# Optimization experiments

Measured on AMD Instinct MI355X. Metric: run time of the kernel, lower is better.

## Reference

```python
import jax, jax.numpy as jnp
import numpy as np

MAXHD, MAXV, MINA, MAXA, DT = 100.0, 40.0, -6.0, 4.0, 0.1
NVEH, NT, IN_DIM, UNITS = 4096, 1024, 12, 20


def setup_inputs() -> dict:
    key = jax.random.key(0)
    ks = jax.random.split(key, 12)
    leadfol_inputs = jax.random.normal(ks[0], (NVEH, NT, IN_DIM), dtype=jnp.float32)
    init_state = jax.random.normal(ks[1], (NVEH, 2), dtype=jnp.float32)
    hidden_states = jnp.zeros((2, NVEH, UNITS), dtype=jnp.float32)
    s = 0.1
    return {
        "leadfol_inputs": leadfol_inputs,
        "init_state": init_state,
        "hidden_states": hidden_states,
        "kernel": s * jax.random.normal(ks[2], (IN_DIM, 4 * UNITS), dtype=jnp.float32),
        "rkernel": s * jax.random.normal(ks[3], (UNITS, 4 * UNITS), dtype=jnp.float32),
        "bias": jnp.zeros((4 * UNITS,), dtype=jnp.float32),
        "W2": s * jax.random.normal(ks[4], (UNITS, 10), dtype=jnp.float32),
        "b2": jnp.zeros((10,), dtype=jnp.float32),
        "Wlc": s * jax.random.normal(ks[5], (10, 3), dtype=jnp.float32),
        "blc": jnp.zeros((3,), dtype=jnp.float32),
        "W1": s * jax.random.normal(ks[6], (10, 1), dtype=jnp.float32),
        "b1": jnp.zeros((1,), dtype=jnp.float32),
    }


def reference(leadfol_inputs, init_state, hidden_states, kernel, rkernel, bias,
              W2, b2, Wlc, blc, W1, b1):
    # time-major for scan: (nt, nveh, 12)
    xs = jnp.transpose(leadfol_inputs, (1, 0, 2))
    pos0, spd0 = init_state[:, 0], init_state[:, 1]
    h0, c0 = hidden_states[0], hidden_states[1]

    def step(carry, x_t):
        pos, spd, h, c = carry
        lead_hd = (x_t[:, :3] - pos[:, None]) / MAXHD
        fol_hd = (pos[:, None] - x_t[:, 3:6]) / MAXHD
        spds = x_t[:, 6:] / MAXV
        inp = jnp.concatenate([lead_hd, fol_hd, spds], axis=1)  # (nveh, 12)
        inp = jnp.where(jnp.isnan(inp), jnp.ones_like(inp), inp)
        # Keras LSTMCell (inference, no dropout): gate order i, f, g, o
        z = inp @ kernel + h @ rkernel + bias
        i_g, f_g, g_g, o_g = jnp.split(z, 4, axis=1)
        c_new = jax.nn.sigmoid(f_g) * c + jax.nn.sigmoid(i_g) * jnp.tanh(g_g)
        h_new = jax.nn.sigmoid(o_g) * jnp.tanh(c_new)
        x2 = jax.nn.relu(h_new @ W2 + b2)          # (nveh, 10)
        lc = x2 @ Wlc + blc                          # (nveh, 3)
        acc_raw = (x2 @ W1 + b1)[:, 0]               # (nveh,)
        acc = (MAXA - MINA) * acc_raw + MINA
        pos_new = pos + DT * spd
        spd_new = spd + DT * acc
        return (pos_new, spd_new, h_new, c_new), (pos_new, lc)

    (pos_f, spd_f, h_f, c_f), (traj, lc_all) = jax.lax.scan(step, (pos0, spd0, h0, c0), xs)
    pred_traj = jnp.transpose(traj, (1, 0))            # (nveh, nt)
    pred_lc_action = jnp.transpose(lc_all, (1, 0, 2))  # (nveh, nt, 3)
    return pred_traj, pred_lc_action, spd_f, (h_f, c_f)
```

## Files before the change

kernel.cpp:

```cpp
#include <hip/hip_runtime.h>
#include <cstdint>

#define NVEH  4096
#define NT    1024
#define INW   12
#define UNITS 20

typedef float f32x2 __attribute__((ext_vector_type(2)));

#define PIN(v)  asm volatile("" : "+v"(v))

#define PKFMA_LO(acc, w, s2) \
    asm("v_pk_fma_f32 %0, %1, %2, %0 op_sel:[0,0,0] op_sel_hi:[1,0,1]" \
        : "+v"(acc) : "v"(w), "v"(s2))
#define PKFMA_HI(acc, w, s2) \
    asm("v_pk_fma_f32 %0, %1, %2, %0 op_sel:[0,1,0] op_sel_hi:[1,1,1]" \
        : "+v"(acc) : "v"(w), "v"(s2))
#define PKMUL_LO(dst, w, s2) \
    asm("v_pk_mul_f32 %0, %1, %2 op_sel:[0,0] op_sel_hi:[1,0]" \
        : "=v"(dst) : "v"(w), "v"(s2))
#define PKFMA(acc, a, b) \
    asm("v_pk_fma_f32 %0, %1, %2, %0" : "+v"(acc) : "v"(a), "v"(b))

__device__ __forceinline__ float fexp2(float x) { return __builtin_amdgcn_exp2f(x); }
__device__ __forceinline__ float frcp(float x)  { return __builtin_amdgcn_rcpf(x); }

__device__ __forceinline__ void gload_lds16(const float* g, float* l) {
    __builtin_amdgcn_global_load_lds(
        (const __attribute__((address_space(1))) unsigned int*)g,
        (__attribute__((address_space(3))) unsigned int*)l,
        16, 0, 0);
}

__global__ __attribute__((amdgpu_waves_per_eu(2, 2))) __launch_bounds__(64)
void rnncf_kernel(const float* __restrict__ x,
                  const float* __restrict__ init_state,
                  const float* __restrict__ hs,
                  const float* __restrict__ K,
                  const float* __restrict__ R,
                  const float* __restrict__ bias,
                  const float* __restrict__ W2,
                  const float* __restrict__ b2,
                  const float* __restrict__ Wlc,
                  const float* __restrict__ blc,
                  const float* __restrict__ W1,
                  const float* __restrict__ b1,
                  float* __restrict__ out)
{
    const int lane = threadIdx.x;
    const int grp  = lane / 20;
    const int sub  = lane % 20;
    const int veh  = blockIdx.x * 3 + grp;
    const bool active = (grp < 3) && (veh < NVEH);
    const int vs = active ? veh : 0;

    __shared__ __align__(16) float x_lds[8][4][12];
    __shared__ __align__(16) float h_lds[4][20];
    __shared__ __align__(16) float x2_lds[4][12];

    const float s01l = -1.4426950408889634f;
    const float s01h = -1.4426950408889634f;
    const float s23l =  2.8853900817779268f;
    const float s23h = -1.4426950408889634f;
    f32x2 K01[12], K23[12], R01[20], R23[20], bz01, bz23;
    bz01[0] = s01l * bias[sub];      bz01[1] = s01h * bias[20 + sub];
    bz23[0] = s23l * bias[40 + sub]; bz23[1] = s23h * bias[60 + sub];
#pragma unroll
    for (int k = 0; k < 12; ++k) {
        K01[k][0] = s01l * K[k * 80 + sub];      K01[k][1] = s01h * K[k * 80 + 20 + sub];
        K23[k][0] = s23l * K[k * 80 + 40 + sub]; K23[k][1] = s23h * K[k * 80 + 60 + sub];
    }
#pragma unroll
    for (int k = 0; k < 20; ++k) {
        R01[k][0] = s01l * R[k * 80 + sub];      R01[k][1] = s01h * R[k * 80 + 20 + sub];
        R23[k][0] = s23l * R[k * 80 + 40 + sub]; R23[k][1] = s23h * R[k * 80 + 60 + sub];
    }
    const int mh = (sub < 10) ? sub : 9;
    f32x2 W2p[10];
#pragma unroll
    for (int u = 0; u < 10; ++u) {
        W2p[u][0] = W2[(2 * u) * 10 + mh];
        W2p[u][1] = W2[(2 * u + 1) * 10 + mh];
    }
    float b2s = b2[mh];
    const int jl = (sub < 3) ? sub : 0;
    f32x2 Wlcp[5];
#pragma unroll
    for (int m = 0; m < 5; ++m) {
        Wlcp[m][0] = Wlc[(2 * m) * 3 + jl];
        Wlcp[m][1] = Wlc[(2 * m + 1) * 3 + jl];
    }
    float blcs = blc[jl];
    f32x2 W1p[5];
#pragma unroll
    for (int m = 0; m < 5; ++m) { W1p[m][0] = W1[2 * m]; W1p[m][1] = W1[2 * m + 1]; }
    PIN(bz01); PIN(bz23);
#pragma unroll
    for (int k = 0; k < 12; ++k) { PIN(K01[k]); PIN(K23[k]); }
#pragma unroll
    for (int k = 0; k < 20; ++k) { PIN(R01[k]); PIN(R23[k]); }
#pragma unroll
    for (int u = 0; u < 10; ++u) PIN(W2p[u]);
#pragma unroll
    for (int m = 0; m < 5; ++m) { PIN(Wlcp[m]); PIN(W1p[m]); }
    PIN(b2s); PIN(blcs);

    float pos = init_state[vs * 2 + 0];
    float spd = init_state[vs * 2 + 1];
    float c   = hs[(size_t)NVEH * UNITS + (size_t)vs * UNITS + sub];
    float hnew = hs[(size_t)vs * UNITS + sub];

    h_lds[grp][sub] = hnew;
    __builtin_amdgcn_wave_barrier();
    f32x2 hrp[10];
#pragma unroll
    for (int q = 0; q < 5; ++q) {
        float4 v = ((const float4*)&h_lds[grp][0])[q];
        hrp[2*q][0]   = v.x; hrp[2*q][1]   = v.y;
        hrp[2*q+1][0] = v.z; hrp[2*q+1][1] = v.w;
    }
    __builtin_amdgcn_wave_barrier();

    const bool stg = (lane < 9);
    int sveh = blockIdx.x * 3 + lane / 3;
    if (sveh > NVEH - 1) sveh = NVEH - 1;
    const float* sgp = x + (size_t)sveh * NT * INW + (lane % 3) * 4;

    if (stg) {
#pragma unroll
        for (int t0 = 0; t0 < 8; ++t0)
            gload_lds16(sgp + (size_t)t0 * INW, &x_lds[t0][0][0]);
    }

    float* trajp = out + (size_t)vs * NT;
    float* lcp   = out + (size_t)NVEH * NT + (size_t)vs * NT * 3;

    float xm = 0.0f;

    for (int tb = 0; tb < NT; tb += 4) {
        asm volatile("s_waitcnt vmcnt(4)" ::: "memory");

#pragma unroll
        for (int j = 0; j < 4; ++j) {
            const int t = tb + j;

            float4 u0 = ((const float4*)&x_lds[t & 7][grp][0])[0];
            float4 u1 = ((const float4*)&x_lds[t & 7][grp][0])[1];
            float4 u2 = ((const float4*)&x_lds[t & 7][grp][0])[2];
            f32x2 x2p[5];
            if (t > 0) {
#pragma unroll
                for (int q = 0; q < 5; ++q)
                    x2p[q] = ((const f32x2*)&x2_lds[grp][0])[q];
            }
            __builtin_amdgcn_wave_barrier();

            const float pp = pos * 0.01f;
            f32x2 inp2[6];
            inp2[0][0] = fmaf(u0.x,  0.01f, -pp); inp2[0][1] = fmaf(u0.y,  0.01f, -pp);
            inp2[1][0] = fmaf(u0.z,  0.01f, -pp); inp2[1][1] = fmaf(u0.w, -0.01f,  pp);
            inp2[2][0] = fmaf(u1.x, -0.01f,  pp); inp2[2][1] = fmaf(u1.y, -0.01f,  pp);
            inp2[3][0] = u1.z * 0.025f;           inp2[3][1] = u1.w * 0.025f;
            inp2[4][0] = u2.x * 0.025f;           inp2[4][1] = u2.y * 0.025f;
            inp2[5][0] = u2.z * 0.025f;           inp2[5][1] = u2.w * 0.025f;

            f32x2 zK01 = bz01, zK23 = bz23;
#pragma unroll
            for (int q = 0; q < 6; ++q) {
                PKFMA_LO(zK01, K01[2*q],   inp2[q]);
                PKFMA_LO(zK23, K23[2*q],   inp2[q]);
                PKFMA_HI(zK01, K01[2*q+1], inp2[q]);
                PKFMA_HI(zK23, K23[2*q+1], inp2[q]);
            }
            f32x2 zA01, zA23, zB01, zB23;
            PKMUL_LO(zA01, R01[0], hrp[0]);
            PKMUL_LO(zA23, R23[0], hrp[0]);
            PKFMA_HI(zA01, R01[1], hrp[0]);
            PKFMA_HI(zA23, R23[1], hrp[0]);
#pragma unroll
            for (int q = 1; q < 5; ++q) {
                PKFMA_LO(zA01, R01[2*q],   hrp[q]);
                PKFMA_LO(zA23, R23[2*q],   hrp[q]);
                PKFMA_HI(zA01, R01[2*q+1], hrp[q]);
                PKFMA_HI(zA23, R23[2*q+1], hrp[q]);
            }
            PKMUL_LO(zB01, R01[10], hrp[5]);
            PKMUL_LO(zB23, R23[10], hrp[5]);
            PKFMA_HI(zB01, R01[11], hrp[5]);
            PKFMA_HI(zB23, R23[11], hrp[5]);
#pragma unroll
            for (int q = 6; q < 10; ++q) {
                PKFMA_LO(zB01, R01[2*q],   hrp[q]);
                PKFMA_LO(zB23, R23[2*q],   hrp[q]);
                PKFMA_HI(zB01, R01[2*q+1], hrp[q]);
                PKFMA_HI(zB23, R23[2*q+1], hrp[q]);
            }
            f32x2 z01 = (zK01 + zA01) + zB01;
            f32x2 z23 = (zK23 + zA23) + zB23;

            if (t > 0) {
                f32x2 ac2; ac2[0] = b1[0]; ac2[1] = 0.0f;
#pragma unroll
                for (int m = 0; m < 5; ++m) PKFMA(ac2, x2p[m], W1p[m]);
                float accr = ac2[0] + ac2[1];
                spd = fmaf(0.1f, fmaf(10.0f, accr, -6.0f), spd);
                if (active && sub < 3) {
                    f32x2 lc2; lc2[0] = blcs; lc2[1] = 0.0f;
#pragma unroll
                    for (int m = 0; m < 5; ++m) PKFMA(lc2, x2p[m], Wlcp[m]);
                    lcp[(t - 1) * 3 + sub] = lc2[0] + lc2[1];
                }
            }

            float ig = frcp(1.0f + fexp2(z01[0]));
            float fg = frcp(1.0f + fexp2(z01[1]));
            float gg = 1.0f - 2.0f * frcp(fexp2(z23[0]) + 1.0f);
            float og = frcp(1.0f + fexp2(z23[1]));
            c = fmaf(fg, c, ig * gg);
            float th = 1.0f - 2.0f * frcp(fexp2(2.8853900817779268f * c) + 1.0f);
            hnew = og * th;

            float posn = fmaf(0.1f, spd, pos);
            if (active && sub == 0) trajp[t] = posn;
            pos = posn;

            h_lds[grp][sub] = hnew;
            __builtin_amdgcn_wave_barrier();
#pragma unroll
            for (int q = 0; q < 5; ++q) {
                float4 v = ((const float4*)&h_lds[grp][0])[q];
                hrp[2*q][0]   = v.x; hrp[2*q][1]   = v.y;
                hrp[2*q+1][0] = v.z; hrp[2*q+1][1] = v.w;
            }
            __builtin_amdgcn_wave_barrier();

            f32x2 xm2; xm2[0] = b2s; xm2[1] = 0.0f;
#pragma unroll
            for (int u = 0; u < 10; ++u) PKFMA(xm2, hrp[u], W2p[u]);
            xm = fmaxf(xm2[0] + xm2[1], 0.0f);
            if (sub < 10) x2_lds[grp][sub] = xm;
            __builtin_amdgcn_wave_barrier();
        }

        if (stg) {
#pragma unroll
            for (int j = 0; j < 4; ++j) {
                int tt = tb + 8 + j; if (tt > NT - 1) tt = NT - 1;
                gload_lds16(sgp + (size_t)tt * INW, &x_lds[(tb + j) & 7][0][0]);
            }
        }
    }

    {
        f32x2 x2p[5];
#pragma unroll
        for (int q = 0; q < 5; ++q)
            x2p[q] = ((const f32x2*)&x2_lds[grp][0])[q];
        f32x2 ac2; ac2[0] = b1[0]; ac2[1] = 0.0f;
#pragma unroll
        for (int m = 0; m < 5; ++m) PKFMA(ac2, x2p[m], W1p[m]);
        float accr = ac2[0] + ac2[1];
        spd = fmaf(0.1f, fmaf(10.0f, accr, -6.0f), spd);
        if (active && sub < 3) {
            f32x2 lc2; lc2[0] = blcs; lc2[1] = 0.0f;
#pragma unroll
            for (int m = 0; m < 5; ++m) PKFMA(lc2, x2p[m], Wlcp[m]);
            lcp[(NT - 1) * 3 + sub] = lc2[0] + lc2[1];
        }
    }

    if (active) {
        float* spdf = out + (size_t)NVEH * NT * 4;
        float* hf   = spdf + NVEH;
        float* cf   = hf + (size_t)NVEH * UNITS;
        if (sub == 0) spdf[veh] = spd;
        hf[(size_t)veh * UNITS + sub] = hnew;
        cf[(size_t)veh * UNITS + sub] = c;
    }
}

extern "C" void kernel_launch(void* const* d_in, const int* in_sizes, int n_in,
                              void* d_out, int out_size, void* d_ws, size_t ws_size,
                              hipStream_t stream) {
    const float* x    = (const float*)d_in[0];
    const float* st0  = (const float*)d_in[1];
    const float* hs   = (const float*)d_in[2];
    const float* K    = (const float*)d_in[3];
    const float* R    = (const float*)d_in[4];
    const float* bias = (const float*)d_in[5];
    const float* W2   = (const float*)d_in[6];
    const float* b2   = (const float*)d_in[7];
    const float* Wlc  = (const float*)d_in[8];
    const float* blc  = (const float*)d_in[9];
    const float* W1   = (const float*)d_in[10];
    const float* b1   = (const float*)d_in[11];
    float* out = (float*)d_out;

    dim3 grid((NVEH + 2) / 3);
    dim3 block(64);
    hipLaunchKernelGGL(rnncf_kernel, grid, block, 0, stream,
                       x, st0, hs, K, R, bias, W2, b2, Wlc, blc, W1, b1, out);
}
```

Baseline: 690.3 us.

## Move input, W2 and Wlc weights to LDS and fold input scaling into kernel

Input-projection weights (with the per-feature scaling and position-difference term folded in), W2 and Wlc now live in shared memory and are read every step, instead of being pinned in registers. W1 is read directly from global (scalar) memory. The point is to cut VGPR pressure, which could raise occupancy, and to drop the per-step input preprocessing arithmetic. In exchange each timestep does more LDS reads on the serial recurrence path, and folding the scale factors into the weights changes floating-point rounding order.

```diff
diff --git a/kernel.cpp b/kernel.cpp
--- a/kernel.cpp
+++ b/kernel.cpp
@@ -57,52 +57,68 @@
     __shared__ __align__(16) float x_lds[8][4][12];
     __shared__ __align__(16) float h_lds[4][20];
     __shared__ __align__(16) float x2_lds[4][12];
+    __shared__ __align__(16) f32x2 ks01l[14][20];
+    __shared__ __align__(16) f32x2 ks23l[14][20];
+    __shared__ __align__(16) f32x2 w2l[10][10];
+    __shared__ __align__(16) f32x2 wlcl[5][3];
 
     const float s01l = -1.4426950408889634f;
     const float s01h = -1.4426950408889634f;
     const float s23l =  2.8853900817779268f;
     const float s23h = -1.4426950408889634f;
-    f32x2 K01[12], K23[12], R01[20], R23[20], bz01, bz23;
-    bz01[0] = s01l * bias[sub];      bz01[1] = s01h * bias[20 + sub];
-    bz23[0] = s23l * bias[40 + sub]; bz23[1] = s23h * bias[60 + sub];
-#pragma unroll
-    for (int k = 0; k < 12; ++k) {
-        K01[k][0] = s01l * K[k * 80 + sub];      K01[k][1] = s01h * K[k * 80 + 20 + sub];
-        K23[k][0] = s23l * K[k * 80 + 40 + sub]; K23[k][1] = s23h * K[k * 80 + 60 + sub];
-    }
+
+    for (int idx = lane; idx < 240; idx += 64) {
+        int k = idx / 20, s = idx % 20;
+        float coef = (k < 3) ? 0.01f : (k < 6) ? -0.01f : 0.025f;
+        f32x2 a, b;
+        a[0] = s01l * coef * K[k * 80 + s];
+        a[1] = s01h * coef * K[k * 80 + 20 + s];
+        b[0] = s23l * coef * K[k * 80 + 40 + s];
+        b[1] = s23h * coef * K[k * 80 + 60 + s];
+        ks01l[k][s] = a; ks23l[k][s] = b;
+    }
+    if (lane < 20) {
+        float a0 = 0, a1 = 0, a2 = 0, a3 = 0;
+        for (int k = 0; k < 6; ++k) {
+            float sgn = (k < 3) ? -0.01f : 0.01f;
+            a0 += sgn * K[k * 80 + lane];
+            a1 += sgn * K[k * 80 + 20 + lane];
+            a2 += sgn * K[k * 80 + 40 + lane];
+            a3 += sgn * K[k * 80 + 60 + lane];
+        }
+        f32x2 kd01, kd23, bz01, bz23;
+        kd01[0] = s01l * a0; kd01[1] = s01h * a1;
+        kd23[0] = s23l * a2; kd23[1] = s23h * a3;
+        bz01[0] = s01l * bias[lane];      bz01[1] = s01h * bias[20 + lane];
+        bz23[0] = s23l * bias[40 + lane]; bz23[1] = s23h * bias[60 + lane];
+        ks01l[13][lane] = kd01; ks23l[13][lane] = kd23;
+        ks01l[12][lane] = bz01; ks23l[12][lane] = bz23;
+    }
+    for (int idx = lane; idx < 100; idx += 64) {
+        int m = idx / 10, u = idx % 10;
+        f32x2 w; w[0] = W2[(2 * u) * 10 + m]; w[1] = W2[(2 * u + 1) * 10 + m];
+        w2l[m][u] = w;
+    }
+    if (lane < 15) {
+        int m = lane / 3, j = lane % 3;
+        f32x2 w; w[0] = Wlc[(2 * m) * 3 + j]; w[1] = Wlc[(2 * m + 1) * 3 + j];
+        wlcl[m][j] = w;
+    }
+    __builtin_amdgcn_wave_barrier();
+
+    f32x2 R01[20], R23[20];
 #pragma unroll
     for (int k = 0; k < 20; ++k) {
         R01[k][0] = s01l * R[k * 80 + sub];      R01[k][1] = s01h * R[k * 80 + 20 + sub];
         R23[k][0] = s23l * R[k * 80 + 40 + sub]; R23[k][1] = s23h * R[k * 80 + 60 + sub];
     }
+#pragma unroll
+    for (int k = 0; k < 20; ++k) { PIN(R01[k]); PIN(R23[k]); }
+
     const int mh = (sub < 10) ? sub : 9;
-    f32x2 W2p[10];
-#pragma unroll
-    for (int u = 0; u < 10; ++u) {
-        W2p[u][0] = W2[(2 * u) * 10 + mh];
-        W2p[u][1] = W2[(2 * u + 1) * 10 + mh];
-    }
-    float b2s = b2[mh];
     const int jl = (sub < 3) ? sub : 0;
-    f32x2 Wlcp[5];
-#pragma unroll
-    for (int m = 0; m < 5; ++m) {
-        Wlcp[m][0] = Wlc[(2 * m) * 3 + jl];
-        Wlcp[m][1] = Wlc[(2 * m + 1) * 3 + jl];
-    }
+    float b2s  = b2[mh];
     float blcs = blc[jl];
-    f32x2 W1p[5];
-#pragma unroll
-    for (int m = 0; m < 5; ++m) { W1p[m][0] = W1[2 * m]; W1p[m][1] = W1[2 * m + 1]; }
-    PIN(bz01); PIN(bz23);
-#pragma unroll
-    for (int k = 0; k < 12; ++k) { PIN(K01[k]); PIN(K23[k]); }
-#pragma unroll
-    for (int k = 0; k < 20; ++k) { PIN(R01[k]); PIN(R23[k]); }
-#pragma unroll
-    for (int u = 0; u < 10; ++u) PIN(W2p[u]);
-#pragma unroll
-    for (int m = 0; m < 5; ++m) { PIN(Wlcp[m]); PIN(W1p[m]); }
     PIN(b2s); PIN(blcs);
 
     float pos = init_state[vs * 2 + 0];
@@ -134,8 +150,6 @@
 
     float* trajp = out + (size_t)vs * NT;
     float* lcp   = out + (size_t)NVEH * NT + (size_t)vs * NT * 3;
-
-    float xm = 0.0f;
 
     for (int tb = 0; tb < NT; tb += 4) {
         asm volatile("s_waitcnt vmcnt(4)" ::: "memory");
@@ -155,23 +169,27 @@
             }
             __builtin_amdgcn_wave_barrier();
 
-            const float pp = pos * 0.01f;
-            f32x2 inp2[6];
-            inp2[0][0] = fmaf(u0.x,  0.01f, -pp); inp2[0][1] = fmaf(u0.y,  0.01f, -pp);
-            inp2[1][0] = fmaf(u0.z,  0.01f, -pp); inp2[1][1] = fmaf(u0.w, -0.01f,  pp);
-            inp2[2][0] = fmaf(u1.x, -0.01f,  pp); inp2[2][1] = fmaf(u1.y, -0.01f,  pp);
-            inp2[3][0] = u1.z * 0.025f;           inp2[3][1] = u1.w * 0.025f;
-            inp2[4][0] = u2.x * 0.025f;           inp2[4][1] = u2.y * 0.025f;
-            inp2[5][0] = u2.z * 0.025f;           inp2[5][1] = u2.w * 0.025f;
-
-            f32x2 zK01 = bz01, zK23 = bz23;
+            f32x2 xp[6];
+            xp[0][0] = u0.x; xp[0][1] = u0.y;
+            xp[1][0] = u0.z; xp[1][1] = u0.w;
+            xp[2][0] = u1.x; xp[2][1] = u1.y;
+            xp[3][0] = u1.z; xp[3][1] = u1.w;
+            xp[4][0] = u2.x; xp[4][1] = u2.y;
+            xp[5][0] = u2.z; xp[5][1] = u2.w;
+
+            f32x2 posp; posp[0] = pos; posp[1] = pos;
+            f32x2 zK01 = ks01l[12][sub] + ks01l[13][sub] * posp;
+            f32x2 zK23 = ks23l[12][sub] + ks23l[13][sub] * posp;
 #pragma unroll
             for (int q = 0; q < 6; ++q) {
-                PKFMA_LO(zK01, K01[2*q],   inp2[q]);
-                PKFMA_LO(zK23, K23[2*q],   inp2[q]);
-                PKFMA_HI(zK01, K01[2*q+1], inp2[q]);
-                PKFMA_HI(zK23, K23[2*q+1], inp2[q]);
-            }
+                f32x2 ka = ks01l[2*q][sub],  kb = ks01l[2*q+1][sub];
+                f32x2 kc = ks23l[2*q][sub],  kd = ks23l[2*q+1][sub];
+                PKFMA_LO(zK01, ka, xp[q]);
+                PKFMA_LO(zK23, kc, xp[q]);
+                PKFMA_HI(zK01, kb, xp[q]);
+                PKFMA_HI(zK23, kd, xp[q]);
+            }
+
             f32x2 zA01, zA23, zB01, zB23;
             PKMUL_LO(zA01, R01[0], hrp[0]);
             PKMUL_LO(zA23, R23[0], hrp[0]);
@@ -199,15 +217,21 @@
             f32x2 z23 = (zK23 + zA23) + zB23;
 
             if (t > 0) {
-                f32x2 ac2; ac2[0] = b1[0]; ac2[1] = 0.0f;
-#pragma unroll
-                for (int m = 0; m < 5; ++m) PKFMA(ac2, x2p[m], W1p[m]);
-                float accr = ac2[0] + ac2[1];
+                float a0 = b1[0], a1 = 0.0f;
+#pragma unroll
+                for (int m = 0; m < 5; ++m) {
+                    a0 = fmaf(x2p[m][0], W1[2*m],   a0);
+                    a1 = fmaf(x2p[m][1], W1[2*m+1], a1);
+                }
+                float accr = a0 + a1;
                 spd = fmaf(0.1f, fmaf(10.0f, accr, -6.0f), spd);
                 if (active && sub < 3) {
                     f32x2 lc2; lc2[0] = blcs; lc2[1] = 0.0f;
 #pragma unroll
-                    for (int m = 0; m < 5; ++m) PKFMA(lc2, x2p[m], Wlcp[m]);
+                    for (int m = 0; m < 5; ++m) {
+                        f32x2 w = wlcl[m][jl];
+                        PKFMA(lc2, x2p[m], w);
+                    }
                     lcp[(t - 1) * 3 + sub] = lc2[0] + lc2[1];
                 }
             }
@@ -236,8 +260,11 @@
 
             f32x2 xm2; xm2[0] = b2s; xm2[1] = 0.0f;
 #pragma unroll
-            for (int u = 0; u < 10; ++u) PKFMA(xm2, hrp[u], W2p[u]);
-            xm = fmaxf(xm2[0] + xm2[1], 0.0f);
+            for (int u = 0; u < 10; ++u) {
+                f32x2 w = w2l[mh][u];
+                PKFMA(xm2, hrp[u], w);
+            }
+            float xm = fmaxf(xm2[0] + xm2[1], 0.0f);
             if (sub < 10) x2_lds[grp][sub] = xm;
             __builtin_amdgcn_wave_barrier();
         }
@@ -256,15 +283,21 @@
 #pragma unroll
         for (int q = 0; q < 5; ++q)
             x2p[q] = ((const f32x2*)&x2_lds[grp][0])[q];
-        f32x2 ac2; ac2[0] = b1[0]; ac2[1] = 0.0f;
-#pragma unroll
-        for (int m = 0; m < 5; ++m) PKFMA(ac2, x2p[m], W1p[m]);
-        float accr = ac2[0] + ac2[1];
+        float a0 = b1[0], a1 = 0.0f;
+#pragma unroll
+        for (int m = 0; m < 5; ++m) {
+            a0 = fmaf(x2p[m][0], W1[2*m],   a0);
+            a1 = fmaf(x2p[m][1], W1[2*m+1], a1);
+        }
+        float accr = a0 + a1;
         spd = fmaf(0.1f, fmaf(10.0f, accr, -6.0f), spd);
         if (active && sub < 3) {
             f32x2 lc2; lc2[0] = blcs; lc2[1] = 0.0f;
 #pragma unroll
-            for (int m = 0; m < 5; ++m) PKFMA(lc2, x2p[m], Wlcp[m]);
+            for (int m = 0; m < 5; ++m) {
+                f32x2 w = wlcl[m][jl];
+                PKFMA(lc2, x2p[m], w);
+            }
             lcp[(NT - 1) * 3 + sub] = lc2[0] + lc2[1];
         }
     }
```

After: 1.131 ms. +63.8%, slower.

## Split recurrent matvec into four accumulation chains and drop wave barriers

Applied to the files above, without the earlier changes.

The recurrent h@R accumulation is split into separate even/odd chains for each half, giving four independent packed-FMA chains per gate pair instead of two. This shortens the serial dependency latency on the critical recurrence path. The wave_barrier calls around LDS exchanges are removed, letting the compiler schedule LDS reads and writes more freely. The W1 weights are now read as uniform scalar loads instead of being pinned in VGPRs, which frees registers. Dropping the barriers risks the compiler reordering LDS accesses within the wave, although the accesses go through memory so ordering should still hold.

```diff
diff --git a/kernel.cpp b/kernel.cpp
--- a/kernel.cpp
+++ b/kernel.cpp
@@ -19,8 +19,9 @@
 #define PKMUL_LO(dst, w, s2) \
     asm("v_pk_mul_f32 %0, %1, %2 op_sel:[0,0] op_sel_hi:[1,0]" \
         : "=v"(dst) : "v"(w), "v"(s2))
-#define PKFMA(acc, a, b) \
-    asm("v_pk_fma_f32 %0, %1, %2, %0" : "+v"(acc) : "v"(a), "v"(b))
+#define PKMUL_HI(dst, w, s2) \
+    asm("v_pk_mul_f32 %0, %1, %2 op_sel:[0,1] op_sel_hi:[1,1]" \
+        : "=v"(dst) : "v"(w), "v"(s2))
 
 __device__ __forceinline__ float fexp2(float x) { return __builtin_amdgcn_exp2f(x); }
 __device__ __forceinline__ float frcp(float x)  { return __builtin_amdgcn_rcpf(x); }
@@ -91,9 +92,6 @@
         Wlcp[m][1] = Wlc[(2 * m + 1) * 3 + jl];
     }
     float blcs = blc[jl];
-    f32x2 W1p[5];
-#pragma unroll
-    for (int m = 0; m < 5; ++m) { W1p[m][0] = W1[2 * m]; W1p[m][1] = W1[2 * m + 1]; }
     PIN(bz01); PIN(bz23);
 #pragma unroll
     for (int k = 0; k < 12; ++k) { PIN(K01[k]); PIN(K23[k]); }
@@ -102,7 +100,7 @@
 #pragma unroll
     for (int u = 0; u < 10; ++u) PIN(W2p[u]);
 #pragma unroll
-    for (int m = 0; m < 5; ++m) { PIN(Wlcp[m]); PIN(W1p[m]); }
+    for (int m = 0; m < 5; ++m) PIN(Wlcp[m]);
     PIN(b2s); PIN(blcs);
 
     float pos = init_state[vs * 2 + 0];
@@ -134,8 +132,6 @@
 
     float* trajp = out + (size_t)vs * NT;
     float* lcp   = out + (size_t)NVEH * NT + (size_t)vs * NT * 3;
-
-    float xm = 0.0f;
 
     for (int tb = 0; tb < NT; tb += 4) {
         asm volatile("s_waitcnt vmcnt(4)" ::: "memory");
@@ -153,7 +149,6 @@
                 for (int q = 0; q < 5; ++q)
                     x2p[q] = ((const f32x2*)&x2_lds[grp][0])[q];
             }
-            __builtin_amdgcn_wave_barrier();
 
             const float pp = pos * 0.01f;
             f32x2 inp2[6];
@@ -172,42 +167,46 @@
                 PKFMA_HI(zK01, K01[2*q+1], inp2[q]);
                 PKFMA_HI(zK23, K23[2*q+1], inp2[q]);
             }
-            f32x2 zA01, zA23, zB01, zB23;
-            PKMUL_LO(zA01, R01[0], hrp[0]);
-            PKMUL_LO(zA23, R23[0], hrp[0]);
-            PKFMA_HI(zA01, R01[1], hrp[0]);
-            PKFMA_HI(zA23, R23[1], hrp[0]);
+            f32x2 cE01, cO01, cE23, cO23;
+            f32x2 dE01, dO01, dE23, dO23;
+            PKMUL_LO(cE01, R01[0], hrp[0]);
+            PKMUL_HI(cO01, R01[1], hrp[0]);
+            PKMUL_LO(cE23, R23[0], hrp[0]);
+            PKMUL_HI(cO23, R23[1], hrp[0]);
+            PKMUL_LO(dE01, R01[10], hrp[5]);
+            PKMUL_HI(dO01, R01[11], hrp[5]);
+            PKMUL_LO(dE23, R23[10], hrp[5]);
+            PKMUL_HI(dO23, R23[11], hrp[5]);
 #pragma unroll
             for (int q = 1; q < 5; ++q) {
-                PKFMA_LO(zA01, R01[2*q],   hrp[q]);
-                PKFMA_LO(zA23, R23[2*q],   hrp[q]);
-                PKFMA_HI(zA01, R01[2*q+1], hrp[q]);
-                PKFMA_HI(zA23, R23[2*q+1], hrp[q]);
-            }
-            PKMUL_LO(zB01, R01[10], hrp[5]);
-            PKMUL_LO(zB23, R23[10], hrp[5]);
-            PKFMA_HI(zB01, R01[11], hrp[5]);
-            PKFMA_HI(zB23, R23[11], hrp[5]);
-#pragma unroll
-            for (int q = 6; q < 10; ++q) {
-                PKFMA_LO(zB01, R01[2*q],   hrp[q]);
-                PKFMA_LO(zB23, R23[2*q],   hrp[q]);
-                PKFMA_HI(zB01, R01[2*q+1], hrp[q]);
-                PKFMA_HI(zB23, R23[2*q+1], hrp[q]);
-            }
-            f32x2 z01 = (zK01 + zA01) + zB01;
-            f32x2 z23 = (zK23 + zA23) + zB23;
+                PKFMA_LO(cE01, R01[2*q],   hrp[q]);
+                PKFMA_HI(cO01, R01[2*q+1], hrp[q]);
+                PKFMA_LO(cE23, R23[2*q],   hrp[q]);
+                PKFMA_HI(cO23, R23[2*q+1], hrp[q]);
+                PKFMA_LO(dE01, R01[2*q+10], hrp[q+5]);
+                PKFMA_HI(dO01, R01[2*q+11], hrp[q+5]);
+                PKFMA_LO(dE23, R23[2*q+10], hrp[q+5]);
+                PKFMA_HI(dO23, R23[2*q+11], hrp[q+5]);
+            }
+            f32x2 z01 = (zK01 + (cE01 + cO01)) + (dE01 + dO01);
+            f32x2 z23 = (zK23 + (cE23 + cO23)) + (dE23 + dO23);
 
             if (t > 0) {
-                f32x2 ac2; ac2[0] = b1[0]; ac2[1] = 0.0f;
-#pragma unroll
-                for (int m = 0; m < 5; ++m) PKFMA(ac2, x2p[m], W1p[m]);
-                float accr = ac2[0] + ac2[1];
+                float a0 = b1[0], a1 = 0.0f;
+#pragma unroll
+                for (int m = 0; m < 5; ++m) {
+                    a0 = fmaf(x2p[m][0], W1[2*m],   a0);
+                    a1 = fmaf(x2p[m][1], W1[2*m+1], a1);
+                }
+                float accr = a0 + a1;
                 spd = fmaf(0.1f, fmaf(10.0f, accr, -6.0f), spd);
                 if (active && sub < 3) {
                     f32x2 lc2; lc2[0] = blcs; lc2[1] = 0.0f;
 #pragma unroll
-                    for (int m = 0; m < 5; ++m) PKFMA(lc2, x2p[m], Wlcp[m]);
+                    for (int m = 0; m < 5; ++m) {
+                        asm("v_pk_fma_f32 %0, %1, %2, %0"
+                            : "+v"(lc2) : "v"(x2p[m]), "v"(Wlcp[m]));
+                    }
                     lcp[(t - 1) * 3 + sub] = lc2[0] + lc2[1];
                 }
             }
@@ -225,21 +224,21 @@
             pos = posn;
 
             h_lds[grp][sub] = hnew;
-            __builtin_amdgcn_wave_barrier();
 #pragma unroll
             for (int q = 0; q < 5; ++q) {
                 float4 v = ((const float4*)&h_lds[grp][0])[q];
                 hrp[2*q][0]   = v.x; hrp[2*q][1]   = v.y;
                 hrp[2*q+1][0] = v.z; hrp[2*q+1][1] = v.w;
             }
-            __builtin_amdgcn_wave_barrier();
 
             f32x2 xm2; xm2[0] = b2s; xm2[1] = 0.0f;
 #pragma unroll
-            for (int u = 0; u < 10; ++u) PKFMA(xm2, hrp[u], W2p[u]);
-            xm = fmaxf(xm2[0] + xm2[1], 0.0f);
+            for (int u = 0; u < 10; ++u) {
+                asm("v_pk_fma_f32 %0, %1, %2, %0"
+                    : "+v"(xm2) : "v"(hrp[u]), "v"(W2p[u]));
+            }
+            float xm = fmaxf(xm2[0] + xm2[1], 0.0f);
             if (sub < 10) x2_lds[grp][sub] = xm;
-            __builtin_amdgcn_wave_barrier();
         }
 
         if (stg) {
@@ -256,15 +255,21 @@
 #pragma unroll
         for (int q = 0; q < 5; ++q)
             x2p[q] = ((const f32x2*)&x2_lds[grp][0])[q];
-        f32x2 ac2; ac2[0] = b1[0]; ac2[1] = 0.0f;
-#pragma unroll
-        for (int m = 0; m < 5; ++m) PKFMA(ac2, x2p[m], W1p[m]);
-        float accr = ac2[0] + ac2[1];
+        float a0 = b1[0], a1 = 0.0f;
+#pragma unroll
+        for (int m = 0; m < 5; ++m) {
+            a0 = fmaf(x2p[m][0], W1[2*m],   a0);
+            a1 = fmaf(x2p[m][1], W1[2*m+1], a1);
+        }
+        float accr = a0 + a1;
         spd = fmaf(0.1f, fmaf(10.0f, accr, -6.0f), spd);
         if (active && sub < 3) {
             f32x2 lc2; lc2[0] = blcs; lc2[1] = 0.0f;
 #pragma unroll
-            for (int m = 0; m < 5; ++m) PKFMA(lc2, x2p[m], Wlcp[m]);
+            for (int m = 0; m < 5; ++m) {
+                asm("v_pk_fma_f32 %0, %1, %2, %0"
+                    : "+v"(lc2) : "v"(x2p[m]), "v"(Wlcp[m]));
+            }
             lcp[(NT - 1) * 3 + sub] = lc2[0] + lc2[1];
         }
     }
```

Result: slower. 716.0 us (+3.7%).

## Process two vehicles per lane pair using packed FMAs over the vehicle dimension

Applied to the files above, without the earlier changes.

Each lane now computes its hidden unit for two vehicles at once. The packed-FMA halves carry vehicle A and vehicle B, and the weight scalar is broadcast with op_sel. This halves the number of blocks (6 vehicles per 64-lane wave) and drops the horizontal reductions in the W2/Wlc paths. Occupancy is lowered to 1 wave per EU to fit the larger register footprint (doubled h, x, and state registers). The trade-off is half as many waves to hide latency, plus a longer serial chain per step.

```diff
diff --git a/kernel.cpp b/kernel.cpp
--- a/kernel.cpp
+++ b/kernel.cpp
@@ -10,17 +10,15 @@
 
 #define PIN(v)  asm volatile("" : "+v"(v))
 
-#define PKFMA_LO(acc, w, s2) \
-    asm("v_pk_fma_f32 %0, %1, %2, %0 op_sel:[0,0,0] op_sel_hi:[1,0,1]" \
-        : "+v"(acc) : "v"(w), "v"(s2))
-#define PKFMA_HI(acc, w, s2) \
-    asm("v_pk_fma_f32 %0, %1, %2, %0 op_sel:[0,1,0] op_sel_hi:[1,1,1]" \
-        : "+v"(acc) : "v"(w), "v"(s2))
-#define PKMUL_LO(dst, w, s2) \
-    asm("v_pk_mul_f32 %0, %1, %2 op_sel:[0,0] op_sel_hi:[1,0]" \
-        : "=v"(dst) : "v"(w), "v"(s2))
-#define PKFMA(acc, a, b) \
-    asm("v_pk_fma_f32 %0, %1, %2, %0" : "+v"(acc) : "v"(a), "v"(b))
+#define PKW_LO(acc, w, d) \
+    asm("v_pk_fma_f32 %0, %1, %2, %0 op_sel:[0,0,0] op_sel_hi:[0,1,1]" \
+        : "+v"(acc) : "v"(w), "v"(d))
+#define PKW_HI(acc, w, d) \
+    asm("v_pk_fma_f32 %0, %1, %2, %0 op_sel:[1,0,0] op_sel_hi:[1,1,1]" \
+        : "+v"(acc) : "v"(w), "v"(d))
+#define PKWMUL_LO(dst, w, d) \
+    asm("v_pk_mul_f32 %0, %1, %2 op_sel:[0,0] op_sel_hi:[0,1]" \
+        : "=v"(dst) : "v"(w), "v"(d))
 
 __device__ __forceinline__ float fexp2(float x) { return __builtin_amdgcn_exp2f(x); }
 __device__ __forceinline__ float frcp(float x)  { return __builtin_amdgcn_rcpf(x); }
@@ -32,7 +30,7 @@
         16, 0, 0);
 }
 
-__global__ __attribute__((amdgpu_waves_per_eu(2, 2))) __launch_bounds__(64)
+__global__ __attribute__((amdgpu_waves_per_eu(1, 1))) __launch_bounds__(64)
 void rnncf_kernel(const float* __restrict__ x,
                   const float* __restrict__ init_state,
                   const float* __restrict__ hs,
@@ -50,79 +48,86 @@
     const int lane = threadIdx.x;
     const int grp  = lane / 20;
     const int sub  = lane % 20;
-    const int veh  = blockIdx.x * 3 + grp;
-    const bool active = (grp < 3) && (veh < NVEH);
-    const int vs = active ? veh : 0;
-
-    __shared__ __align__(16) float x_lds[8][4][12];
-    __shared__ __align__(16) float h_lds[4][20];
-    __shared__ __align__(16) float x2_lds[4][12];
-
-    const float s01l = -1.4426950408889634f;
-    const float s01h = -1.4426950408889634f;
-    const float s23l =  2.8853900817779268f;
-    const float s23h = -1.4426950408889634f;
-    f32x2 K01[12], K23[12], R01[20], R23[20], bz01, bz23;
-    bz01[0] = s01l * bias[sub];      bz01[1] = s01h * bias[20 + sub];
-    bz23[0] = s23l * bias[40 + sub]; bz23[1] = s23h * bias[60 + sub];
-#pragma unroll
-    for (int k = 0; k < 12; ++k) {
-        K01[k][0] = s01l * K[k * 80 + sub];      K01[k][1] = s01h * K[k * 80 + 20 + sub];
-        K23[k][0] = s23l * K[k * 80 + 40 + sub]; K23[k][1] = s23h * K[k * 80 + 60 + sub];
-    }
-#pragma unroll
-    for (int k = 0; k < 20; ++k) {
-        R01[k][0] = s01l * R[k * 80 + sub];      R01[k][1] = s01h * R[k * 80 + 20 + sub];
-        R23[k][0] = s23l * R[k * 80 + 40 + sub]; R23[k][1] = s23h * R[k * 80 + 60 + sub];
+    const int gc   = (grp < 3) ? grp : 2;
+    const int vA   = blockIdx.x * 6 + gc * 2;
+    const int vB   = vA + 1;
+    const bool aA  = (grp < 3) && (vA < NVEH);
+    const bool aB  = (grp < 3) && (vB < NVEH);
+    const int vsA  = (vA < NVEH) ? vA : NVEH - 1;
+    const int vsB  = (vB < NVEH) ? vB : NVEH - 1;
+
+    __shared__ __align__(16) float x_lds[8][6][12];
+    __shared__ __align__(16) f32x2 h_lds[3][20];
+    __shared__ __align__(16) f32x2 x2_lds[3][10];
+
+    const float L2E = 1.4426950408889634f;
+    f32x2 Kp[4][6], Rp[4][10], bz2[4];
+#pragma unroll
+    for (int g = 0; g < 4; ++g) {
+        const float s = (g == 2) ? (2.0f * L2E) : (-L2E);
+        bz2[g][0] = bz2[g][1] = s * bias[g * 20 + sub];
+#pragma unroll
+        for (int kp = 0; kp < 6; ++kp) {
+            Kp[g][kp][0] = s * K[(2 * kp)     * 80 + g * 20 + sub];
+            Kp[g][kp][1] = s * K[(2 * kp + 1) * 80 + g * 20 + sub];
+        }
+#pragma unroll
+        for (int kp = 0; kp < 10; ++kp) {
+            Rp[g][kp][0] = s * R[(2 * kp)     * 80 + g * 20 + sub];
+            Rp[g][kp][1] = s * R[(2 * kp + 1) * 80 + g * 20 + sub];
+        }
     }
     const int mh = (sub < 10) ? sub : 9;
     f32x2 W2p[10];
 #pragma unroll
-    for (int u = 0; u < 10; ++u) {
-        W2p[u][0] = W2[(2 * u) * 10 + mh];
-        W2p[u][1] = W2[(2 * u + 1) * 10 + mh];
-    }
-    float b2s = b2[mh];
+    for (int up = 0; up < 10; ++up) {
+        W2p[up][0] = W2[(2 * up)     * 10 + mh];
+        W2p[up][1] = W2[(2 * up + 1) * 10 + mh];
+    }
+    f32x2 b2s2; b2s2[0] = b2s2[1] = b2[mh];
     const int jl = (sub < 3) ? sub : 0;
     f32x2 Wlcp[5];
 #pragma unroll
-    for (int m = 0; m < 5; ++m) {
-        Wlcp[m][0] = Wlc[(2 * m) * 3 + jl];
-        Wlcp[m][1] = Wlc[(2 * m + 1) * 3 + jl];
+    for (int mp = 0; mp < 5; ++mp) {
+        Wlcp[mp][0] = Wlc[(2 * mp)     * 3 + jl];
+        Wlcp[mp][1] = Wlc[(2 * mp + 1) * 3 + jl];
     }
     float blcs = blc[jl];
-    f32x2 W1p[5];
-#pragma unroll
-    for (int m = 0; m < 5; ++m) { W1p[m][0] = W1[2 * m]; W1p[m][1] = W1[2 * m + 1]; }
-    PIN(bz01); PIN(bz23);
-#pragma unroll
-    for (int k = 0; k < 12; ++k) { PIN(K01[k]); PIN(K23[k]); }
-#pragma unroll
-    for (int k = 0; k < 20; ++k) { PIN(R01[k]); PIN(R23[k]); }
-#pragma unroll
-    for (int u = 0; u < 10; ++u) PIN(W2p[u]);
-#pragma unroll
-    for (int m = 0; m < 5; ++m) { PIN(Wlcp[m]); PIN(W1p[m]); }
-    PIN(b2s); PIN(blcs);
-
-    float pos = init_state[vs * 2 + 0];
-    float spd = init_state[vs * 2 + 1];
-    float c   = hs[(size_t)NVEH * UNITS + (size_t)vs * UNITS + sub];
-    float hnew = hs[(size_t)vs * UNITS + sub];
-
-    h_lds[grp][sub] = hnew;
+#pragma unroll
+    for (int g = 0; g < 4; ++g) {
+        PIN(bz2[g]);
+#pragma unroll
+        for (int kp = 0; kp < 6; ++kp)  PIN(Kp[g][kp]);
+#pragma unroll
+        for (int kp = 0; kp < 10; ++kp) PIN(Rp[g][kp]);
+    }
+#pragma unroll
+    for (int up = 0; up < 10; ++up) PIN(W2p[up]);
+#pragma unroll
+    for (int mp = 0; mp < 5; ++mp)  PIN(Wlcp[mp]);
+    PIN(b2s2); PIN(blcs);
+
+    f32x2 pos2, spd2, c2, hnew2;
+    pos2[0] = init_state[vsA * 2 + 0]; pos2[1] = init_state[vsB * 2 + 0];
+    spd2[0] = init_state[vsA * 2 + 1]; spd2[1] = init_state[vsB * 2 + 1];
+    c2[0]   = hs[(size_t)NVEH * UNITS + (size_t)vsA * UNITS + sub];
+    c2[1]   = hs[(size_t)NVEH * UNITS + (size_t)vsB * UNITS + sub];
+    hnew2[0] = hs[(size_t)vsA * UNITS + sub];
+    hnew2[1] = hs[(size_t)vsB * UNITS + sub];
+
+    if (grp < 3) h_lds[grp][sub] = hnew2;
     __builtin_amdgcn_wave_barrier();
-    f32x2 hrp[10];
-#pragma unroll
-    for (int q = 0; q < 5; ++q) {
-        float4 v = ((const float4*)&h_lds[grp][0])[q];
-        hrp[2*q][0]   = v.x; hrp[2*q][1]   = v.y;
-        hrp[2*q+1][0] = v.z; hrp[2*q+1][1] = v.w;
+    f32x2 hrp2[20];
+#pragma unroll
+    for (int q = 0; q < 10; ++q) {
+        float4 v = ((const float4*)&h_lds[gc][0])[q];
+        hrp2[2*q][0]   = v.x; hrp2[2*q][1]   = v.y;
+        hrp2[2*q+1][0] = v.z; hrp2[2*q+1][1] = v.w;
     }
     __builtin_amdgcn_wave_barrier();
 
-    const bool stg = (lane < 9);
-    int sveh = blockIdx.x * 3 + lane / 3;
+    const bool stg = (lane < 18);
+    int sveh = blockIdx.x * 6 + lane / 3;
     if (sveh > NVEH - 1) sveh = NVEH - 1;
     const float* sgp = x + (size_t)sveh * NT * INW + (lane % 3) * 4;
 
@@ -132,10 +137,10 @@
             gload_lds16(sgp + (size_t)t0 * INW, &x_lds[t0][0][0]);
     }
 
-    float* trajp = out + (size_t)vs * NT;
-    float* lcp   = out + (size_t)NVEH * NT + (size_t)vs * NT * 3;
-
-    float xm = 0.0f;
+    float* trajpA = out + (size_t)vsA * NT;
+    float* trajpB = out + (size_t)vsB * NT;
+    float* lcpA   = out + (size_t)NVEH * NT + (size_t)vsA * NT * 3;
+    float* lcpB   = out + (size_t)NVEH * NT + (size_t)vsB * NT * 3;
 
     for (int tb = 0; tb < NT; tb += 4) {
         asm volatile("s_waitcnt vmcnt(4)" ::: "memory");
@@ -144,101 +149,129 @@
         for (int j = 0; j < 4; ++j) {
             const int t = tb + j;
 
-            float4 u0 = ((const float4*)&x_lds[t & 7][grp][0])[0];
-            float4 u1 = ((const float4*)&x_lds[t & 7][grp][0])[1];
-            float4 u2 = ((const float4*)&x_lds[t & 7][grp][0])[2];
-            f32x2 x2p[5];
+            const float4* xba = (const float4*)&x_lds[t & 7][gc * 2][0];
+            const float4* xbb = (const float4*)&x_lds[t & 7][gc * 2 + 1][0];
+            float4 uA0 = xba[0], uA1 = xba[1], uA2 = xba[2];
+            float4 uB0 = xbb[0], uB1 = xbb[1], uB2 = xbb[2];
+            f32x2 x2p[10];
             if (t > 0) {
 #pragma unroll
-                for (int q = 0; q < 5; ++q)
-                    x2p[q] = ((const f32x2*)&x2_lds[grp][0])[q];
+                for (int q = 0; q < 5; ++q) {
+                    float4 v = ((const float4*)&x2_lds[gc][0])[q];
+                    x2p[2*q][0]   = v.x; x2p[2*q][1]   = v.y;
+                    x2p[2*q+1][0] = v.z; x2p[2*q+1][1] = v.w;
+                }
             }
             __builtin_amdgcn_wave_barrier();
 
-            const float pp = pos * 0.01f;
-            f32x2 inp2[6];
-            inp2[0][0] = fmaf(u0.x,  0.01f, -pp); inp2[0][1] = fmaf(u0.y,  0.01f, -pp);
-            inp2[1][0] = fmaf(u0.z,  0.01f, -pp); inp2[1][1] = fmaf(u0.w, -0.01f,  pp);
-            inp2[2][0] = fmaf(u1.x, -0.01f,  pp); inp2[2][1] = fmaf(u1.y, -0.01f,  pp);
-            inp2[3][0] = u1.z * 0.025f;           inp2[3][1] = u1.w * 0.025f;
-            inp2[4][0] = u2.x * 0.025f;           inp2[4][1] = u2.y * 0.025f;
-            inp2[5][0] = u2.z * 0.025f;           inp2[5][1] = u2.w * 0.025f;
-
-            f32x2 zK01 = bz01, zK23 = bz23;
-#pragma unroll
-            for (int q = 0; q < 6; ++q) {
-                PKFMA_LO(zK01, K01[2*q],   inp2[q]);
-                PKFMA_LO(zK23, K23[2*q],   inp2[q]);
-                PKFMA_HI(zK01, K01[2*q+1], inp2[q]);
-                PKFMA_HI(zK23, K23[2*q+1], inp2[q]);
-            }
-            f32x2 zA01, zA23, zB01, zB23;
-            PKMUL_LO(zA01, R01[0], hrp[0]);
-            PKMUL_LO(zA23, R23[0], hrp[0]);
-            PKFMA_HI(zA01, R01[1], hrp[0]);
-            PKFMA_HI(zA23, R23[1], hrp[0]);
-#pragma unroll
-            for (int q = 1; q < 5; ++q) {
-                PKFMA_LO(zA01, R01[2*q],   hrp[q]);
-                PKFMA_LO(zA23, R23[2*q],   hrp[q]);
-                PKFMA_HI(zA01, R01[2*q+1], hrp[q]);
-                PKFMA_HI(zA23, R23[2*q+1], hrp[q]);
-            }
-            PKMUL_LO(zB01, R01[10], hrp[5]);
-            PKMUL_LO(zB23, R23[10], hrp[5]);
-            PKFMA_HI(zB01, R01[11], hrp[5]);
-            PKFMA_HI(zB23, R23[11], hrp[5]);
-#pragma unroll
-            for (int q = 6; q < 10; ++q) {
-                PKFMA_LO(zB01, R01[2*q],   hrp[q]);
-                PKFMA_LO(zB23, R23[2*q],   hrp[q]);
-                PKFMA_HI(zB01, R01[2*q+1], hrp[q]);
-                PKFMA_HI(zB23, R23[2*q+1], hrp[q]);
-            }
-            f32x2 z01 = (zK01 + zA01) + zB01;
-            f32x2 z23 = (zK23 + zA23) + zB23;
+            const float ppA = pos2[0] * 0.01f, ppB = pos2[1] * 0.01f;
+            f32x2 inp2[12];
+            inp2[0][0]  = fmaf(uA0.x,  0.01f, -ppA); inp2[0][1]  = fmaf(uB0.x,  0.01f, -ppB);
+            inp2[1][0]  = fmaf(uA0.y,  0.01f, -ppA); inp2[1][1]  = fmaf(uB0.y,  0.01f, -ppB);
+            inp2[2][0]  = fmaf(uA0.z,  0.01f, -ppA); inp2[2][1]  = fmaf(uB0.z,  0.01f, -ppB);
+            inp2[3][0]  = fmaf(uA0.w, -0.01f,  ppA); inp2[3][1]  = fmaf(uB0.w, -0.01f,  ppB);
+            inp2[4][0]  = fmaf(uA1.x, -0.01f,  ppA); inp2[4][1]  = fmaf(uB1.x, -0.01f,  ppB);
+            inp2[5][0]  = fmaf(uA1.y, -0.01f,  ppA); inp2[5][1]  = fmaf(uB1.y, -0.01f,  ppB);
+            inp2[6][0]  = uA1.z * 0.025f;            inp2[6][1]  = uB1.z * 0.025f;
+            inp2[7][0]  = uA1.w * 0.025f;            inp2[7][1]  = uB1.w * 0.025f;
+            inp2[8][0]  = uA2.x * 0.025f;            inp2[8][1]  = uB2.x * 0.025f;
+            inp2[9][0]  = uA2.y * 0.025f;            inp2[9][1]  = uB2.y * 0.025f;
+            inp2[10][0] = uA2.z * 0.025f;            inp2[10][1] = uB2.z * 0.025f;
+            inp2[11][0] = uA2.w * 0.025f;            inp2[11][1] = uB2.w * 0.025f;
+
+            f32x2 zK[4], zA[4], zB[4];
+#pragma unroll
+            for (int g = 0; g < 4; ++g) {
+                zK[g] = bz2[g];
+#pragma unroll
+                for (int kp = 0; kp < 6; ++kp) {
+                    PKW_LO(zK[g], Kp[g][kp], inp2[2*kp]);
+                    PKW_HI(zK[g], Kp[g][kp], inp2[2*kp+1]);
+                }
+            }
+#pragma unroll
+            for (int g = 0; g < 4; ++g) {
+                PKWMUL_LO(zA[g], Rp[g][0], hrp2[0]);
+                PKW_HI   (zA[g], Rp[g][0], hrp2[1]);
+#pragma unroll
+                for (int kp = 1; kp < 5; ++kp) {
+                    PKW_LO(zA[g], Rp[g][kp], hrp2[2*kp]);
+                    PKW_HI(zA[g], Rp[g][kp], hrp2[2*kp+1]);
+                }
+                PKWMUL_LO(zB[g], Rp[g][5], hrp2[10]);
+                PKW_HI   (zB[g], Rp[g][5], hrp2[11]);
+#pragma unroll
+                for (int kp = 6; kp < 10; ++kp) {
+                    PKW_LO(zB[g], Rp[g][kp], hrp2[2*kp]);
+                    PKW_HI(zB[g], Rp[g][kp], hrp2[2*kp+1]);
+                }
+            }
+            f32x2 z0 = (zK[0] + zA[0]) + zB[0];
+            f32x2 z1 = (zK[1] + zA[1]) + zB[1];
+            f32x2 z2 = (zK[2] + zA[2]) + zB[2];
+            f32x2 z3 = (zK[3] + zA[3]) + zB[3];
 
             if (t > 0) {
-                f32x2 ac2; ac2[0] = b1[0]; ac2[1] = 0.0f;
-#pragma unroll
-                for (int m = 0; m < 5; ++m) PKFMA(ac2, x2p[m], W1p[m]);
-                float accr = ac2[0] + ac2[1];
-                spd = fmaf(0.1f, fmaf(10.0f, accr, -6.0f), spd);
-                if (active && sub < 3) {
-                    f32x2 lc2; lc2[0] = blcs; lc2[1] = 0.0f;
-#pragma unroll
-                    for (int m = 0; m < 5; ++m) PKFMA(lc2, x2p[m], Wlcp[m]);
-                    lcp[(t - 1) * 3 + sub] = lc2[0] + lc2[1];
-                }
-            }
-
-            float ig = frcp(1.0f + fexp2(z01[0]));
-            float fg = frcp(1.0f + fexp2(z01[1]));
-            float gg = 1.0f - 2.0f * frcp(fexp2(z23[0]) + 1.0f);
-            float og = frcp(1.0f + fexp2(z23[1]));
-            c = fmaf(fg, c, ig * gg);
-            float th = 1.0f - 2.0f * frcp(fexp2(2.8853900817779268f * c) + 1.0f);
-            hnew = og * th;
-
-            float posn = fmaf(0.1f, spd, pos);
-            if (active && sub == 0) trajp[t] = posn;
-            pos = posn;
-
-            h_lds[grp][sub] = hnew;
+                float a0 = b1[0], a1 = b1[0];
+#pragma unroll
+                for (int m = 0; m < 10; ++m) {
+                    a0 = fmaf(x2p[m][0], W1[m], a0);
+                    a1 = fmaf(x2p[m][1], W1[m], a1);
+                }
+                spd2[0] = fmaf(0.1f, fmaf(10.0f, a0, -6.0f), spd2[0]);
+                spd2[1] = fmaf(0.1f, fmaf(10.0f, a1, -6.0f), spd2[1]);
+                if (grp < 3 && sub < 3) {
+                    f32x2 lc2; lc2[0] = blcs; lc2[1] = blcs;
+#pragma unroll
+                    for (int mp = 0; mp < 5; ++mp) {
+                        PKW_LO(lc2, Wlcp[mp], x2p[2*mp]);
+                        PKW_HI(lc2, Wlcp[mp], x2p[2*mp+1]);
+                    }
+                    if (aA) lcpA[(t - 1) * 3 + sub] = lc2[0];
+                    if (aB) lcpB[(t - 1) * 3 + sub] = lc2[1];
+                }
+            }
+
+            f32x2 ig2, fg2, gg2, og2;
+            ig2[0] = frcp(1.0f + fexp2(z0[0])); ig2[1] = frcp(1.0f + fexp2(z0[1]));
+            fg2[0] = frcp(1.0f + fexp2(z1[0])); fg2[1] = frcp(1.0f + fexp2(z1[1]));
+            gg2[0] = 1.0f - 2.0f * frcp(fexp2(z2[0]) + 1.0f);
+            gg2[1] = 1.0f - 2.0f * frcp(fexp2(z2[1]) + 1.0f);
+            og2[0] = frcp(1.0f + fexp2(z3[0])); og2[1] = frcp(1.0f + fexp2(z3[1]));
+            c2 = fg2 * c2 + ig2 * gg2;
+            f32x2 th2;
+            th2[0] = 1.0f - 2.0f * frcp(fexp2(2.8853900817779268f * c2[0]) + 1.0f);
+            th2[1] = 1.0f - 2.0f * frcp(fexp2(2.8853900817779268f * c2[1]) + 1.0f);
+            hnew2 = og2 * th2;
+
+            f32x2 posn2 = pos2;
+            posn2[0] = fmaf(0.1f, spd2[0], pos2[0]);
+            posn2[1] = fmaf(0.1f, spd2[1], pos2[1]);
+            if (sub == 0) {
+                if (aA) trajpA[t] = posn2[0];
+                if (aB) trajpB[t] = posn2[1];
+            }
+            pos2 = posn2;
+
+            if (grp < 3) h_lds[grp][sub] = hnew2;
             __builtin_amdgcn_wave_barrier();
 #pragma unroll
-            for (int q = 0; q < 5; ++q) {
-                float4 v = ((const float4*)&h_lds[grp][0])[q];
-                hrp[2*q][0]   = v.x; hrp[2*q][1]   = v.y;
-                hrp[2*q+1][0] = v.z; hrp[2*q+1][1] = v.w;
+            for (int q = 0; q < 10; ++q) {
+                float4 v = ((const float4*)&h_lds[gc][0])[q];
+                hrp2[2*q][0]   = v.x; hrp2[2*q][1]   = v.y;
+                hrp2[2*q+1][0] = v.z; hrp2[2*q+1][1] = v.w;
             }
             __builtin_amdgcn_wave_barrier();
 
-            f32x2 xm2; xm2[0] = b2s; xm2[1] = 0.0f;
-#pragma unroll
-            for (int u = 0; u < 10; ++u) PKFMA(xm2, hrp[u], W2p[u]);
-            xm = fmaxf(xm2[0] + xm2[1], 0.0f);
-            if (sub < 10) x2_lds[grp][sub] = xm;
+            f32x2 xm2 = b2s2;
+#pragma unroll
+            for (int up = 0; up < 10; ++up) {
+                PKW_LO(xm2, W2p[up], hrp2[2*up]);
+                PKW_HI(xm2, W2p[up], hrp2[2*up+1]);
+            }
+            xm2[0] = fmaxf(xm2[0], 0.0f);
+            xm2[1] = fmaxf(xm2[1], 0.0f);
+            if (grp < 3 && sub < 10) x2_lds[grp][sub] = xm2;
             __builtin_amdgcn_wave_barrier();
         }
 
@@ -252,30 +285,49 @@
     }
 
     {
-        f32x2 x2p[5];
-#pragma unroll
-        for (int q = 0; q < 5; ++q)
-            x2p[q] = ((const f32x2*)&x2_lds[grp][0])[q];
-        f32x2 ac2; ac2[0] = b1[0]; ac2[1] = 0.0f;
-#pragma unroll
-        for (int m = 0; m < 5; ++m) PKFMA(ac2, x2p[m], W1p[m]);
-        float accr = ac2[0] + ac2[1];
-        spd = fmaf(0.1f, fmaf(10.0f, accr, -6.0f), spd);
-        if (active && sub < 3) {
-            f32x2 lc2; lc2[0] = blcs; lc2[1] = 0.0f;
-#pragma unroll
-            for (int m = 0; m < 5; ++m) PKFMA(lc2, x2p[m], Wlcp[m]);
-            lcp[(NT - 1) * 3 + sub] = lc2[0] + lc2[1];
-        }
-    }
-
-    if (active) {
+        f32x2 x2p[10];
+#pragma unroll
+        for (int q = 0; q < 5; ++q) {
+            float4 v = ((const float4*)&x2_lds[gc][0])[q];
+            x2p[2*q][0]   = v.x; x2p[2*q][1]   = v.y;
+            x2p[2*q+1][0] = v.z; x2p[2*q+1][1] = v.w;
+        }
+        float a0 = b1[0], a1 = b1[0];
+#pragma unroll
+        for (int m = 0; m < 10; ++m) {
+            a0 = fmaf(x2p[m][0], W1[m], a0);
+            a1 = fmaf(x2p[m][1], W1[m], a1);
+        }
+        spd2[0] = fmaf(0.1f, fmaf(10.0f, a0, -6.0f), spd2[0]);
+        spd2[1] = fmaf(0.1f, fmaf(10.0f, a1, -6.0f), spd2[1]);
+        if (grp < 3 && sub < 3) {
+            f32x2 lc2; lc2[0] = blcs; lc2[1] = blcs;
+#pragma unroll
+            for (int mp = 0; mp < 5; ++mp) {
+                PKW_LO(lc2, Wlcp[mp], x2p[2*mp]);
+                PKW_HI(lc2, Wlcp[mp], x2p[2*mp+1]);
+            }
+            if (aA) lcpA[(NT - 1) * 3 + sub] = lc2[0];
+            if (aB) lcpB[(NT - 1) * 3 + sub] = lc2[1];
+        }
+    }
+
+    {
         float* spdf = out + (size_t)NVEH * NT * 4;
         float* hf   = spdf + NVEH;
         float* cf   = hf + (size_t)NVEH * UNITS;
-        if (sub == 0) spdf[veh] = spd;
-        hf[(size_t)veh * UNITS + sub] = hnew;
-        cf[(size_t)veh * UNITS + sub] = c;
+        if (sub == 0) {
+            if (aA) spdf[vA] = spd2[0];
+            if (aB) spdf[vB] = spd2[1];
+        }
+        if (aA) {
+            hf[(size_t)vA * UNITS + sub] = hnew2[0];
+            cf[(size_t)vA * UNITS + sub] = c2[0];
+        }
+        if (aB) {
+            hf[(size_t)vB * UNITS + sub] = hnew2[1];
+            cf[(size_t)vB * UNITS + sub] = c2[1];
+        }
     }
 }
 
@@ -296,7 +348,7 @@
     const float* b1   = (const float*)d_in[11];
     float* out = (float*)d_out;
 
-    dim3 grid((NVEH + 2) / 3);
+    dim3 grid((NVEH + 5) / 6);
     dim3 block(64);
     hipLaunchKernelGGL(rnncf_kernel, grid, block, 0, stream,
                        x, st0, hs, K, R, bias, W2, b2, Wlc, blc, W1, b1, out);
```

Result: slower. 983.0 us (+42.4%).
